# Performance work log

Measured on AMD Instinct MI355X. Metric: run time of the kernel, lower is better.

Reference implementation:

```python
import jax, jax.numpy as jnp
import numpy as np

B, H, W, C = 2, 128, 128, 128
K = 3            # window_size
NB = K * K       # neighbor_count = 9
RP = 8           # relative_position_dim
HID = 128        # edge hidden = max(256//2, 128)
EIN = 3 * C + RP # edge_input_dim = 392
CLIP = 3.0
GEPS = 1e-06     # gate_eps
LNE = 1e-05      # LayerNorm eps


def _ln(x, g, b):
    m = x.mean(-1, keepdims=True)
    v = ((x - m) ** 2).mean(-1, keepdims=True)
    return (x - m) * jax.lax.rsqrt(v + LNE) * g + b


def setup_inputs() -> dict:
    key = jax.random.key(0)
    ks = jax.random.split(key, 12)
    f32 = jnp.float32
    inp = {
        'tokens': jax.random.normal(ks[0], (B, H, W, C), dtype=f32),
        'ln1_g': jnp.ones((C,), f32), 'ln1_b': jnp.zeros((C,), f32),
        'ln2_g': jnp.ones((C,), f32), 'ln2_b': jnp.zeros((C,), f32),
        'rel_pos': 0.02 * jax.random.normal(ks[1], (NB, RP), dtype=f32),
        'dW1': 0.01 * jax.random.normal(ks[2], (EIN, HID), dtype=f32),
        'db1': jnp.zeros((HID,), f32),
        'dW2': 0.01 * jax.random.normal(ks[3], (HID, 1), dtype=f32),
        'db2': jnp.zeros((1,), f32),
        'rW1': 0.01 * jax.random.normal(ks[4], (EIN, HID), dtype=f32),
        'rb1': jnp.zeros((HID,), f32),
        'rW2': 0.01 * jax.random.normal(ks[5], (HID, 1), dtype=f32),
        'rb2': jnp.zeros((1,), f32),
        'vW': 0.01 * jax.random.normal(ks[6], (C, C), dtype=f32),
        'vb': jnp.zeros((C,), f32),
        'oW': 0.01 * jax.random.normal(ks[7], (C, C), dtype=f32),
        'ob': jnp.zeros((C,), f32),
        'eml_gamma': jnp.asarray(0.1, f32),
        'eml_lam': jnp.asarray(1.0, f32),
        'eml_bias': jnp.asarray(-0.3, f32),
    }
    return inp


def _edge_mlp(x, W1, b1, W2, b2):
    h = jax.nn.gelu(jnp.einsum('blnd,dh->blnh', x, W1) + b1, approximate=False)
    return jnp.einsum('blnh,ho->blno', h, W2) + b2


def _forward(tokens, ln1_g, ln1_b, ln2_g, ln2_b, rel_pos, dW1, db1, dW2, db2,
             rW1, rb1, rW2, rb2, vW, vb, oW, ob, eml_gamma, eml_lam, eml_bias,
             warmup_eta=1.0):
    Bh, Hh, Wh, Ch = tokens.shape
    L = Hh * Wh
    normalized = _ln(tokens, ln1_g, ln1_b)
    flat = normalized.reshape(Bh, L, Ch)
    # Unfold(kernel=3, padding=1): gather 9 shifted views, then replicate torch's
    # reshape of the (C, 9)-ordered channel axis into (9, C).
    pad = jnp.pad(normalized, ((0, 0), (1, 1), (1, 1), (0, 0)))
    shifts = [pad[:, i:i + Hh, j:j + Wh, :] for i in range(K) for j in range(K)]
    nbhd = jnp.stack(shifts, axis=-1)                       # [B,H,W,C,9]
    nbhd = nbhd.reshape(Bh, L, Ch * NB).reshape(Bh, L, NB, Ch)  # torch reshape semantics
    center = jnp.broadcast_to(flat[:, :, None, :], nbhd.shape)
    rel = jnp.broadcast_to(rel_pos[None, None], (Bh, L, NB, rel_pos.shape[-1]))
    edge_features = jnp.concatenate([center, nbhd, center - nbhd, rel], axis=-1)
    drive = _edge_mlp(edge_features, dW1, db1, dW2, db2)[..., 0]        # [B,L,9]
    resistance = _edge_mlp(edge_features, rW1, rb1, rW2, rb2)[..., 0]   # [B,L,9]
    # EML unit (Ohm's-law style gate): clamp(eta*gamma*drive/(lambda*softplus(R)+eps)+bias)
    energy = jnp.clip(
        warmup_eta * (eml_gamma * drive) / (eml_lam * jax.nn.softplus(resistance) + GEPS)
        + eml_bias, -CLIP, CLIP)
    gate = jax.nn.sigmoid(energy)                                        # [B,L,9]
    values = jnp.einsum('blnc,cd->blnd', nbhd, vW) + vb                  # [B,L,9,C]
    gate_mass = jnp.maximum(gate.sum(axis=2), GEPS)                      # [B,L]
    message = jnp.einsum('bln,blnc->blc', gate, values) / gate_mass[..., None]
    update = (jnp.einsum('blc,cd->bld', message, oW) + ob).reshape(Bh, Hh, Wh, Ch)
    output = _ln(tokens + update, ln2_g, ln2_b)  # dropout is identity at eval
    return output


def reference(tokens, ln1_g, ln1_b, ln2_g, ln2_b, rel_pos, dW1, db1, dW2, db2,
              rW1, rb1, rW2, rb2, vW, vb, oW, ob, eml_gamma, eml_lam, eml_bias):
    return _forward(tokens, ln1_g, ln1_b, ln2_g, ln2_b, rel_pos, dW1, db1, dW2, db2,
                    rW1, rb1, rW2, rb2, vW, vb, oW, ob, eml_gamma, eml_lam, eml_bias)
```

## Files before the change

### kernel.cpp

```cpp
#include <hip/hip_runtime.h>


#define USHORT unsigned short
#define AW 152

typedef __attribute__((ext_vector_type(8)))  __bf16 v8bf;
typedef __attribute__((ext_vector_type(8)))  USHORT v8u;
typedef __attribute__((ext_vector_type(16))) float  v16f;

__device__ __forceinline__ USHORT f2bf(float f) {
    unsigned v; __builtin_memcpy(&v, &f, 4);
    v += 0x7FFFu + ((v >> 16) & 1u);
    return (USHORT)(v >> 16);
}

__global__ __launch_bounds__(256) void k_setup(
    const float* __restrict__ tok, const float* __restrict__ ln1g,
    const float* __restrict__ ln1b,
    const float* __restrict__ dW1, const float* __restrict__ db1,
    const float* __restrict__ rW1, const float* __restrict__ rb1,
    const float* __restrict__ rel, const float* __restrict__ dW2,
    const float* __restrict__ rW2, const float* __restrict__ vW,
    const float* __restrict__ vb,  const float* __restrict__ oW,
    USHORT* __restrict__ norm,
    USHORT* __restrict__ WnTg, USHORT* __restrict__ WcTg, USHORT* __restrict__ VTg,
    float* __restrict__ preg, float* __restrict__ vboWg, float* __restrict__ w2g)
{
    const int blk = blockIdx.x, t = threadIdx.x;
    if (blk >= 354) {
        const int p = (blk - 354) * 4 + (t >> 6);
        const int lane = t & 63;
        const float2 x = ((const float2*)(tok + (size_t)p * 128))[lane];
        float s = x.x + x.y;
        for (int m = 1; m < 64; m <<= 1) s += __shfl_xor(s, m);
        const float mean = s * (1.f / 128.f);
        const float d0 = x.x - mean, d1 = x.y - mean;
        float q = d0 * d0 + d1 * d1;
        for (int m = 1; m < 64; m <<= 1) q += __shfl_xor(q, m);
        const float rstd = rsqrtf(q * (1.f / 128.f) + 1e-5f);
        const float2 gg = ((const float2*)ln1g)[lane], bb = ((const float2*)ln1b)[lane];
        ((unsigned*)norm)[(size_t)p * 64 + lane] =
            (unsigned)f2bf(d0 * rstd * gg.x + bb.x) |
            ((unsigned)f2bf(d1 * rstd * gg.y + bb.y) << 16);
        return;
    }
    if (blk < 72) {
        int idx = blk * 256 + t;
        int n = ((idx >> 4) * 7282) >> 16;
        int k = idx - n * 144;
        int r = k >> 4, tt = k & 15, c2 = r + 9 * tt;
        float acc = 0.f;
        if (c2 < 128)
            for (int j = 0; j < 128; ++j) acc += vW[c2 * 128 + j] * oW[j * 128 + n];
        VTg[idx] = f2bf(acc);
    } else if (blk < 216) {
        int idx = (blk - 72) * 256 + t;
        int n = ((idx >> 4) * 7282) >> 16;
        int k = idx - n * 144;
        int r = k >> 4, tt = k & 15, c2 = r + 9 * tt;
        int col = n & 127;
        const float* W = (n < 128) ? dW1 : rW1;
        float val = 0.f;
        if (c2 < 128) val = W[(128 + c2) * 128 + col] - W[(256 + c2) * 128 + col];
        WnTg[idx] = f2bf(val);
    } else if (blk < 344) {
        int idx = (blk - 216) * 256 + t;
        int n = idx >> 7, c = idx & 127, col = n & 127;
        const float* W = (n < 128) ? dW1 : rW1;
        WcTg[idx] = f2bf(W[c * 128 + col] + W[(256 + c) * 128 + col]);
    } else if (blk < 353) {
        int n2 = blk - 344; int h = t;
        float acc;
        if (h < 128) {
            acc = db1[h];
            for (int r = 0; r < 8; ++r) acc += rel[n2 * 8 + r] * dW1[(384 + r) * 128 + h];
        } else {
            int hh = h - 128;
            acc = rb1[hh];
            for (int r = 0; r < 8; ++r) acc += rel[n2 * 8 + r] * rW1[(384 + r) * 128 + hh];
        }
        preg[n2 * 256 + h] = acc;
    } else {
        if (t < 128) {
            float acc = 0.f;
            for (int j = 0; j < 128; ++j) acc += vb[j] * oW[j * 128 + t];
            vboWg[t] = acc;
            w2g[t] = dW2[t];
            w2g[128 + t] = rW2[t];
        }
    }
}

__device__ __forceinline__ void gather_tile(
    USHORT* __restrict__ Ash, const USHORT* __restrict__ nb,
    int n2, int y, int bI, int tid)
{
    const int x = tid >> 2, q = tid & 3;
    #pragma unroll
    for (int r = 0; r < 9; ++r) {
        int u = 2 * n2 + r;
        int n = (u >= 18) ? (u - 18) : ((u >= 9) ? (u - 9) : u);
        int v = n2 * 128 + r;
        int c0 = (v * 7282) >> 16;
        int dyq = (n * 22) >> 6;
        int dx = n - 3 * dyq - 1;
        int dy = dyq - 1;
        int sy = y + dy, sx = x + dx;
        bool ok = ((unsigned)sy < 128u) && ((unsigned)sx < 128u);
        int e0 = (c0 & ~1) + 4 * q;
        size_t gidx = ((size_t)((bI * 128 + (ok ? sy : 0)) * 128 + (ok ? sx : 0))) * 128 + e0;
        const unsigned* gp = (const unsigned*)nb + (gidx >> 1);
        unsigned dw0 = gp[0], dw1 = gp[1];
        unsigned nxt = (unsigned)__shfl_down((int)dw0, 1);
        unsigned o0, o1;
        if (c0 & 1) { o0 = (dw0 >> 16) | (dw1 << 16); o1 = (dw1 >> 16) | (nxt << 16); }
        else        { o0 = dw0;                       o1 = dw1; }
        if (!ok) { o0 = 0u; o1 = 0u; }
        *(uint2*)(Ash + x * AW + 16 * r + 4 * q) = make_uint2(o0, o1);
    }
}

__global__ __launch_bounds__(512, 2) void k_edge(
    const float* __restrict__ tok, const float* __restrict__ ln2g,
    const float* __restrict__ ln2b, const USHORT* __restrict__ nb,
    const USHORT* __restrict__ WnTg, const USHORT* __restrict__ WcTg,
    const USHORT* __restrict__ VTg, const float* __restrict__ preg,
    const float* __restrict__ vboWg, const float* __restrict__ w2g,
    const float* __restrict__ db2p, const float* __restrict__ rb2p,
    const float* __restrict__ gmp, const float* __restrict__ lmp,
    const float* __restrict__ bip, const float* __restrict__ obp,
    float* __restrict__ out)
{
    extern __shared__ char smem[];
    USHORT* Wsh  = (USHORT*)smem;
    USHORT* Ash  = (USHORT*)(smem + 77824);
    USHORT* VTl  = (USHORT*)(smem + 116736);
    float*  w2L  = (float*)(smem + 155648);
    float*  dsum = (float*)(smem + 156672);
    float*  rsum = (float*)(smem + 157184);
    float*  gateL= (float*)(smem + 157696);
    float*  sgL  = (float*)(smem + 158208);
    float*  updF = (float*)smem;

    const int tid = threadIdx.x;
    const int lane = tid & 63, wave = tid >> 6, hi = lane >> 5, l31 = lane & 31;
    const int mw = wave & 1, nw = wave >> 1;
    const int blk = blockIdx.x;
    const int bI = blk >> 7;
    const int y = ((blk & 7) << 4) | ((blk >> 3) & 15);
    const int p0 = (bI * 128 + y) * 128;

    for (int i = tid; i < 4096; i += 512) {
        int n = i >> 4, kv = i & 15;
        *(v8u*)(Wsh + n * AW + kv * 8) = *(const v8u*)(WcTg + n * 128 + kv * 8);
    }
    for (int i = tid; i < 2048; i += 512) {
        int x = i >> 4, kv = i & 15;
        *(v8u*)(Ash + x * AW + kv * 8) = *(const v8u*)(nb + (size_t)(p0 + x) * 128 + kv * 8);
    }
    for (int i = tid; i < 2304; i += 512) {
        int n = (i * 3641) >> 16;
        int kv = i - n * 18;
        *(v8u*)(VTl + n * AW + kv * 8) = *(const v8u*)(VTg + n * 144 + kv * 8);
    }
    if (tid < 256) w2L[tid] = w2g[tid];
    if (tid < 128) { dsum[tid] = 0.f; rsum[tid] = 0.f; sgL[tid] = 0.f; }
    __syncthreads();

    v16f cp[2][2];
    #pragma unroll
    for (int a = 0; a < 2; ++a)
        for (int b = 0; b < 2; ++b)
            for (int e = 0; e < 16; ++e) cp[a][b][e] = 0.f;
    #pragma unroll
    for (int ks = 0; ks < 8; ++ks) {
        v8bf af0 = *(const v8bf*)(Ash + (mw * 64 + l31) * AW + ks * 16 + hi * 8);
        v8bf af1 = *(const v8bf*)(Ash + (mw * 64 + 32 + l31) * AW + ks * 16 + hi * 8);
        v8bf bf0 = *(const v8bf*)(Wsh + (nw * 64 + l31) * AW + ks * 16 + hi * 8);
        v8bf bf1 = *(const v8bf*)(Wsh + (nw * 64 + 32 + l31) * AW + ks * 16 + hi * 8);
        cp[0][0] = __builtin_amdgcn_mfma_f32_32x32x16_bf16(af0, bf0, cp[0][0], 0, 0, 0);
        cp[0][1] = __builtin_amdgcn_mfma_f32_32x32x16_bf16(af0, bf1, cp[0][1], 0, 0, 0);
        cp[1][0] = __builtin_amdgcn_mfma_f32_32x32x16_bf16(af1, bf0, cp[1][0], 0, 0, 0);
        cp[1][1] = __builtin_amdgcn_mfma_f32_32x32x16_bf16(af1, bf1, cp[1][1], 0, 0, 0);
    }
    __syncthreads();

    for (int i = tid; i < 4608; i += 512) {
        int n = (i * 3641) >> 16;
        int kv = i - n * 18;
        *(v8u*)(Wsh + n * AW + kv * 8) = *(const v8u*)(WnTg + n * 144 + kv * 8);
    }
    gather_tile(Ash, nb, 0, y, bI, tid);

    const float gmv = gmp[0], lmv = lmp[0], biv = bip[0];
    const float db2v = db2p[0], rb2v = rb2p[0];
    const float wv0 = w2L[nw * 64 + l31];
    const float wv1 = w2L[nw * 64 + 32 + l31];

    v16f acc3[2];
    #pragma unroll
    for (int a = 0; a < 2; ++a)
        for (int e = 0; e < 16; ++e) acc3[a][e] = 0.f;

    for (int n2 = 0; n2 < 9; ++n2) {
        const float pv0 = preg[n2 * 256 + nw * 64 + l31];
        const float pv1 = preg[n2 * 256 + nw * 64 + 32 + l31];
        __syncthreads();
        v16f acc[2][2];
        #pragma unroll
        for (int a = 0; a < 2; ++a)
            for (int b = 0; b < 2; ++b) acc[a][b] = cp[a][b];
        #pragma unroll
        for (int ks = 0; ks < 9; ++ks) {
            v8bf af0 = *(const v8bf*)(Ash + (mw * 64 + l31) * AW + ks * 16 + hi * 8);
            v8bf af1 = *(const v8bf*)(Ash + (mw * 64 + 32 + l31) * AW + ks * 16 + hi * 8);
            v8bf bf0 = *(const v8bf*)(Wsh + (nw * 64 + l31) * AW + ks * 16 + hi * 8);
            v8bf bf1 = *(const v8bf*)(Wsh + (nw * 64 + 32 + l31) * AW + ks * 16 + hi * 8);
            acc[0][0] = __builtin_amdgcn_mfma_f32_32x32x16_bf16(af0, bf0, acc[0][0], 0, 0, 0);
            acc[0][1] = __builtin_amdgcn_mfma_f32_32x32x16_bf16(af0, bf1, acc[0][1], 0, 0, 0);
            acc[1][0] = __builtin_amdgcn_mfma_f32_32x32x16_bf16(af1, bf0, acc[1][0], 0, 0, 0);
            acc[1][1] = __builtin_amdgcn_mfma_f32_32x32x16_bf16(af1, bf1, acc[1][1], 0, 0, 0);
        }
        #pragma unroll
        for (int mt = 0; mt < 2; ++mt) {
            float part[16];
            #pragma unroll
            for (int rr = 0; rr < 16; ++rr) {
                float h0 = acc[mt][0][rr] + pv0;
                float h1 = acc[mt][1][rr] + pv1;
                float s0 = __builtin_amdgcn_rcpf(1.f + __expf(-1.702f * h0));
                float s1 = __builtin_amdgcn_rcpf(1.f + __expf(-1.702f * h1));
                part[rr] = h0 * s0 * wv0 + h1 * s1 * wv1;
            }
            #pragma unroll
            for (int m = 1; m < 32; m <<= 1) {
                #pragma unroll
                for (int rr = 0; rr < 16; ++rr) part[rr] += __shfl_xor(part[rr], m);
            }
            if (l31 == 0) {
                float* tgt = (nw < 2) ? dsum : rsum;
                #pragma unroll
                for (int rr = 0; rr < 16; ++rr) {
                    int row = mw * 64 + mt * 32 + (rr & 3) + 8 * (rr >> 2) + 4 * hi;
                    atomicAdd(&tgt[row], part[rr]);
                }
            }
        }
        v16f P[2];
        #pragma unroll
        for (int a = 0; a < 2; ++a)
            for (int e = 0; e < 16; ++e) P[a][e] = 0.f;
        #pragma unroll
        for (int ks = 0; ks < 9; ++ks) {
            v8bf af0 = *(const v8bf*)(Ash + (mw * 64 + l31) * AW + ks * 16 + hi * 8);
            v8bf af1 = *(const v8bf*)(Ash + (mw * 64 + 32 + l31) * AW + ks * 16 + hi * 8);
            v8bf vf  = *(const v8bf*)(VTl + (nw * 32 + l31) * AW + ks * 16 + hi * 8);
            P[0] = __builtin_amdgcn_mfma_f32_32x32x16_bf16(af0, vf, P[0], 0, 0, 0);
            P[1] = __builtin_amdgcn_mfma_f32_32x32x16_bf16(af1, vf, P[1], 0, 0, 0);
        }
        __syncthreads();
        if (n2 < 8) gather_tile(Ash, nb, n2 + 1, y, bI, tid);
        if (tid < 128) {
            float d = dsum[tid] + db2v, rr = rsum[tid] + rb2v;
            float sp = fmaxf(rr, 0.f) + log1pf(__expf(-fabsf(rr)));
            float e = gmv * d / (lmv * sp + 1e-6f) + biv;
            e = fminf(fmaxf(e, -3.f), 3.f);
            float gt = 1.f / (1.f + __expf(-e));
            gateL[tid] = gt; sgL[tid] += gt;
            dsum[tid] = 0.f; rsum[tid] = 0.f;
        }
        __syncthreads();
        #pragma unroll
        for (int mt = 0; mt < 2; ++mt) {
            const float4* gq = (const float4*)&gateL[mw * 64 + mt * 32 + 4 * hi];
            float4 ga = gq[0], gb = gq[2], gc = gq[4], gd = gq[6];
            float gs[16] = {ga.x, ga.y, ga.z, ga.w, gb.x, gb.y, gb.z, gb.w,
                            gc.x, gc.y, gc.z, gc.w, gd.x, gd.y, gd.z, gd.w};
            #pragma unroll
            for (int rr = 0; rr < 16; ++rr) acc3[mt][rr] += gs[rr] * P[mt][rr];
        }
    }

    if (tid < 128) {
        float s = sgL[tid];
        float m = fmaxf(s, 1e-6f);
        dsum[tid] = 1.f / m;
        rsum[tid] = s / m;
    }
    __syncthreads();

    {
        const int colc = nw * 32 + l31;
        const float vbw = vboWg[colc], obv = obp[colc];
        #pragma unroll
        for (int mt = 0; mt < 2; ++mt) {
            const int base = mw * 64 + mt * 32 + 4 * hi;
            const float4* iq = (const float4*)&dsum[base];
            const float4* sq = (const float4*)&rsum[base];
            float4 ia = iq[0], ib = iq[2], ic = iq[4], id = iq[6];
            float4 sa = sq[0], sb = sq[2], sc = sq[4], sd = sq[6];
            float iv[16] = {ia.x, ia.y, ia.z, ia.w, ib.x, ib.y, ib.z, ib.w,
                            ic.x, ic.y, ic.z, ic.w, id.x, id.y, id.z, id.w};
            float sv[16] = {sa.x, sa.y, sa.z, sa.w, sb.x, sb.y, sb.z, sb.w,
                            sc.x, sc.y, sc.z, sc.w, sd.x, sd.y, sd.z, sd.w};
            #pragma unroll
            for (int rr = 0; rr < 16; ++rr) {
                int row = base + (rr & 3) + 8 * (rr >> 2);
                updF[row * 128 + colc] = acc3[mt][rr] * iv[rr] + vbw * sv[rr] + obv;
            }
        }
    }
    __syncthreads();

    const float g20 = ln2g[lane], g21 = ln2g[lane + 64];
    const float b20 = ln2b[lane], b21 = ln2b[lane + 64];
    for (int q2 = 0; q2 < 16; ++q2) {
        int p = wave * 16 + q2;
        size_t gp = (size_t)(p0 + p) * 128;
        float x0 = tok[gp + lane]      + updF[p * 128 + lane];
        float x1 = tok[gp + lane + 64] + updF[p * 128 + lane + 64];
        float s = x0 + x1;
        for (int m = 1; m < 64; m <<= 1) s += __shfl_xor(s, m);
        float mean = s * (1.f / 128.f);
        float d0 = x0 - mean, d1 = x1 - mean;
        float qq = d0 * d0 + d1 * d1;
        for (int m = 1; m < 64; m <<= 1) qq += __shfl_xor(qq, m);
        float rstd = rsqrtf(qq * (1.f / 128.f) + 1e-5f);
        out[gp + lane]      = d0 * rstd * g20 + b20;
        out[gp + lane + 64] = d1 * rstd * g21 + b21;
    }
}

extern "C" void kernel_launch(void* const* d_in, const int* in_sizes, int n_in,
                              void* d_out, int out_size, void* d_ws, size_t ws_size,
                              hipStream_t stream) {
    const float* tok  = (const float*)d_in[0];
    const float* ln1g = (const float*)d_in[1];
    const float* ln1b = (const float*)d_in[2];
    const float* ln2g = (const float*)d_in[3];
    const float* ln2b = (const float*)d_in[4];
    const float* rel  = (const float*)d_in[5];
    const float* dW1  = (const float*)d_in[6];
    const float* db1  = (const float*)d_in[7];
    const float* dW2  = (const float*)d_in[8];
    const float* db2  = (const float*)d_in[9];
    const float* rW1  = (const float*)d_in[10];
    const float* rb1  = (const float*)d_in[11];
    const float* rW2  = (const float*)d_in[12];
    const float* rb2  = (const float*)d_in[13];
    const float* vW   = (const float*)d_in[14];
    const float* vb   = (const float*)d_in[15];
    const float* oW   = (const float*)d_in[16];
    const float* ob   = (const float*)d_in[17];
    const float* gm   = (const float*)d_in[18];
    const float* lm   = (const float*)d_in[19];
    const float* bi   = (const float*)d_in[20];
    float* out = (float*)d_out;

    char* w = (char*)d_ws;
    USHORT* norm = (USHORT*)w; w += 8388608;
    USHORT* WnTg = (USHORT*)w; w += 73728;
    USHORT* WcTg = (USHORT*)w; w += 65536;
    USHORT* VTg  = (USHORT*)w; w += 36864;
    float*  preg = (float*)w;  w += 9216;
    float*  vboWg= (float*)w;  w += 512;
    float*  w2g  = (float*)w;  w += 1024;

    hipFuncSetAttribute((const void*)k_edge,
                        hipFuncAttributeMaxDynamicSharedMemorySize, 158720);

    hipLaunchKernelGGL(k_setup, dim3(8546), dim3(256), 0, stream,
                       tok, ln1g, ln1b, dW1, db1, rW1, rb1, rel, dW2, rW2,
                       vW, vb, oW, norm, WnTg, WcTg, VTg, preg, vboWg, w2g);
    hipLaunchKernelGGL(k_edge, dim3(256), dim3(512), 158720, stream,
                       tok, ln2g, ln2b, norm, WnTg, WcTg, VTg, preg, vboWg, w2g,
                       db2, rb2, gm, lm, bi, ob, out);
}
```

Before: 209.8 us.

## Double edge kernel workgroup to 1024 threads and fuse value GEMM into edge loop

The edge kernel now runs 16 waves per workgroup with 32x32 output tiles per wave. Each wave computes the drive, resistance and value MFMAs in one pass over a combined weight buffer in shared memory. Sums are double-buffered, which removes one barrier per neighbor step, and the next neighbor gather is loaded into registers before the barrier so it overlaps compute. The setup kernel is reorganised so that more threads are active and it zero-fills the padding slots. The change adds more atomics per row and lowers per-wave register headroom, and occupancy is limited by the roughly 155KB of shared memory per workgroup.

```diff
diff --git a/kernel.cpp b/kernel.cpp
--- a/kernel.cpp
+++ b/kernel.cpp
@@ -8,6 +8,12 @@
 typedef __attribute__((ext_vector_type(8)))  USHORT v8u;
 typedef __attribute__((ext_vector_type(16))) float  v16f;
 
+__device__ __forceinline__ float bflo(unsigned u) {
+    unsigned v = u << 16; float f; __builtin_memcpy(&f, &v, 4); return f;
+}
+__device__ __forceinline__ float bfhi(unsigned u) {
+    unsigned v = u & 0xffff0000u; float f; __builtin_memcpy(&f, &v, 4); return f;
+}
 __device__ __forceinline__ USHORT f2bf(float f) {
     unsigned v; __builtin_memcpy(&v, &f, 4);
     v += 0x7FFFu + ((v >> 16) & 1u);
@@ -27,8 +33,8 @@
     float* __restrict__ preg, float* __restrict__ vboWg, float* __restrict__ w2g)
 {
     const int blk = blockIdx.x, t = threadIdx.x;
-    if (blk >= 354) {
-        const int p = (blk - 354) * 4 + (t >> 6);
+    if (blk < 8192) {
+        const int p = blk * 4 + (t >> 6);
         const int lane = t & 63;
         const float2 x = ((const float2*)(tok + (size_t)p * 128))[lane];
         float s = x.x + x.y;
@@ -44,32 +50,28 @@
             ((unsigned)f2bf(d1 * rstd * gg.y + bb.y) << 16);
         return;
     }
-    if (blk < 72) {
-        int idx = blk * 256 + t;
-        int n = ((idx >> 4) * 7282) >> 16;
-        int k = idx - n * 144;
-        int r = k >> 4, tt = k & 15, c2 = r + 9 * tt;
+    const int b2 = blk - 8192;
+    if (b2 < 64) {
+        int c2 = b2 * 2 + (t >> 7);
+        int n = t & 127;
         float acc = 0.f;
-        if (c2 < 128)
-            for (int j = 0; j < 128; ++j) acc += vW[c2 * 128 + j] * oW[j * 128 + n];
-        VTg[idx] = f2bf(acc);
-    } else if (blk < 216) {
-        int idx = (blk - 72) * 256 + t;
-        int n = ((idx >> 4) * 7282) >> 16;
-        int k = idx - n * 144;
-        int r = k >> 4, tt = k & 15, c2 = r + 9 * tt;
-        int col = n & 127;
+        for (int j = 0; j < 128; ++j) acc += vW[c2 * 128 + j] * oW[j * 128 + n];
+        int tt = (c2 * 7282) >> 16, r = c2 - 9 * tt;
+        VTg[n * 144 + 16 * r + tt] = f2bf(acc);
+    } else if (b2 < 192) {
+        int c2 = b2 - 64;
+        int n = t, col = t & 127;
         const float* W = (n < 128) ? dW1 : rW1;
-        float val = 0.f;
-        if (c2 < 128) val = W[(128 + c2) * 128 + col] - W[(256 + c2) * 128 + col];
-        WnTg[idx] = f2bf(val);
-    } else if (blk < 344) {
-        int idx = (blk - 216) * 256 + t;
-        int n = idx >> 7, c = idx & 127, col = n & 127;
+        float val = W[(128 + c2) * 128 + col] - W[(256 + c2) * 128 + col];
+        int tt = (c2 * 7282) >> 16, r = c2 - 9 * tt;
+        WnTg[n * 144 + 16 * r + tt] = f2bf(val);
+    } else if (b2 < 320) {
+        int c = b2 - 192;
+        int n = t, col = t & 127;
         const float* W = (n < 128) ? dW1 : rW1;
-        WcTg[idx] = f2bf(W[c * 128 + col] + W[(256 + c) * 128 + col]);
-    } else if (blk < 353) {
-        int n2 = blk - 344; int h = t;
+        WcTg[n * 128 + c] = f2bf(W[c * 128 + col] + W[(256 + c) * 128 + col]);
+    } else if (b2 < 329) {
+        int n2 = b2 - 320; int h = t;
         float acc;
         if (h < 128) {
             acc = db1[h];
@@ -80,7 +82,7 @@
             for (int r = 0; r < 8; ++r) acc += rel[n2 * 8 + r] * rW1[(384 + r) * 128 + hh];
         }
         preg[n2 * 256 + h] = acc;
-    } else {
+    } else if (b2 == 329) {
         if (t < 128) {
             float acc = 0.f;
             for (int j = 0; j < 128; ++j) acc += vb[j] * oW[j * 128 + t];
@@ -88,14 +90,26 @@
             w2g[t] = dW2[t];
             w2g[128 + t] = rW2[t];
         }
-    }
-}
-
-__device__ __forceinline__ void gather_tile(
-    USHORT* __restrict__ Ash, const USHORT* __restrict__ nb,
-    int n2, int y, int bI, int tid)
+    } else {
+        for (int i = t; i < 2048; i += 256) {
+            int n = i >> 4, j = i & 15;
+            int slot = (j == 0) ? 15 : (j == 1) ? 31
+                      : 16 * (2 + ((j - 2) >> 1)) + 14 + ((j - 2) & 1);
+            VTg[n * 144 + slot] = 0;
+        }
+        for (int i = t; i < 4096; i += 256) {
+            int n = i >> 4, j = i & 15;
+            int slot = (j == 0) ? 15 : (j == 1) ? 31
+                      : 16 * (2 + ((j - 2) >> 1)) + 14 + ((j - 2) & 1);
+            WnTg[n * 144 + slot] = 0;
+        }
+    }
+}
+
+__device__ __forceinline__ void gather_load(
+    unsigned gv[9], const USHORT* __restrict__ nb,
+    int n2, int y, int bI, int x, int q)
 {
-    const int x = tid >> 2, q = tid & 3;
     #pragma unroll
     for (int r = 0; r < 9; ++r) {
         int u = 2 * n2 + r;
@@ -103,24 +117,26 @@
         int v = n2 * 128 + r;
         int c0 = (v * 7282) >> 16;
         int dyq = (n * 22) >> 6;
-        int dx = n - 3 * dyq - 1;
-        int dy = dyq - 1;
+        int dx = n - 3 * dyq - 1, dy = dyq - 1;
         int sy = y + dy, sx = x + dx;
         bool ok = ((unsigned)sy < 128u) && ((unsigned)sx < 128u);
-        int e0 = (c0 & ~1) + 4 * q;
+        int e0 = (c0 & ~1) + 2 * q;
         size_t gidx = ((size_t)((bI * 128 + (ok ? sy : 0)) * 128 + (ok ? sx : 0))) * 128 + e0;
-        const unsigned* gp = (const unsigned*)nb + (gidx >> 1);
-        unsigned dw0 = gp[0], dw1 = gp[1];
-        unsigned nxt = (unsigned)__shfl_down((int)dw0, 1);
-        unsigned o0, o1;
-        if (c0 & 1) { o0 = (dw0 >> 16) | (dw1 << 16); o1 = (dw1 >> 16) | (nxt << 16); }
-        else        { o0 = dw0;                       o1 = dw1; }
-        if (!ok) { o0 = 0u; o1 = 0u; }
-        *(uint2*)(Ash + x * AW + 16 * r + 4 * q) = make_uint2(o0, o1);
-    }
-}
-
-__global__ __launch_bounds__(512, 2) void k_edge(
+        unsigned dw = ((const unsigned*)nb)[gidx >> 1];
+        unsigned nxt = (unsigned)__shfl_down((int)dw, 1);
+        unsigned o = (c0 & 1) ? ((dw >> 16) | (nxt << 16)) : dw;
+        gv[r] = ok ? o : 0u;
+    }
+}
+__device__ __forceinline__ void gather_store(
+    USHORT* __restrict__ Ash, const unsigned gv[9], int x, int q)
+{
+    #pragma unroll
+    for (int r = 0; r < 9; ++r)
+        *(unsigned*)(Ash + x * AW + 16 * r + 2 * q) = gv[r];
+}
+
+__global__ __launch_bounds__(1024, 4) void k_edge(
     const float* __restrict__ tok, const float* __restrict__ ln2g,
     const float* __restrict__ ln2b, const USHORT* __restrict__ nb,
     const USHORT* __restrict__ WnTg, const USHORT* __restrict__ WcTg,
@@ -132,190 +148,166 @@
     float* __restrict__ out)
 {
     extern __shared__ char smem[];
-    USHORT* Wsh  = (USHORT*)smem;
-    USHORT* Ash  = (USHORT*)(smem + 77824);
-    USHORT* VTl  = (USHORT*)(smem + 116736);
-    float*  w2L  = (float*)(smem + 155648);
-    float*  dsum = (float*)(smem + 156672);
-    float*  rsum = (float*)(smem + 157184);
-    float*  gateL= (float*)(smem + 157696);
-    float*  sgL  = (float*)(smem + 158208);
+    USHORT* Wp   = (USHORT*)smem;
+    USHORT* Ash  = (USHORT*)(smem + 116736);
+    float*  sums = (float*)(smem + 155648);
+    float*  sgL  = sums + 512;
     float*  updF = (float*)smem;
 
     const int tid = threadIdx.x;
     const int lane = tid & 63, wave = tid >> 6, hi = lane >> 5, l31 = lane & 31;
-    const int mw = wave & 1, nw = wave >> 1;
+    const int mw = wave & 3, nw = wave >> 2;
+    const int gx = tid >> 3, gq = tid & 7;
     const int blk = blockIdx.x;
     const int bI = blk >> 7;
     const int y = ((blk & 7) << 4) | ((blk >> 3) & 15);
     const int p0 = (bI * 128 + y) * 128;
 
-    for (int i = tid; i < 4096; i += 512) {
+    for (int i = tid; i < 4096; i += 1024) {
         int n = i >> 4, kv = i & 15;
-        *(v8u*)(Wsh + n * AW + kv * 8) = *(const v8u*)(WcTg + n * 128 + kv * 8);
-    }
-    for (int i = tid; i < 2048; i += 512) {
+        *(v8u*)(Wp + n * AW + kv * 8) = *(const v8u*)(WcTg + n * 128 + kv * 8);
+    }
+    for (int i = tid; i < 2048; i += 1024) {
         int x = i >> 4, kv = i & 15;
         *(v8u*)(Ash + x * AW + kv * 8) = *(const v8u*)(nb + (size_t)(p0 + x) * 128 + kv * 8);
     }
-    for (int i = tid; i < 2304; i += 512) {
+    if (tid < 640) sums[tid] = 0.f;
+    __syncthreads();
+
+    v16f c0a, c1a;
+    #pragma unroll
+    for (int e = 0; e < 16; ++e) { c0a[e] = 0.f; c1a[e] = 0.f; }
+    #pragma unroll
+    for (int ks = 0; ks < 8; ++ks) {
+        v8bf a  = *(const v8bf*)(Ash + (mw * 32 + l31) * AW + ks * 16 + hi * 8);
+        v8bf b0 = *(const v8bf*)(Wp + (nw * 32 + l31) * AW + ks * 16 + hi * 8);
+        v8bf b1 = *(const v8bf*)(Wp + (128 + nw * 32 + l31) * AW + ks * 16 + hi * 8);
+        c0a = __builtin_amdgcn_mfma_f32_32x32x16_bf16(a, b0, c0a, 0, 0, 0);
+        c1a = __builtin_amdgcn_mfma_f32_32x32x16_bf16(a, b1, c1a, 0, 0, 0);
+    }
+    unsigned cpk[16];
+    #pragma unroll
+    for (int e = 0; e < 16; ++e)
+        cpk[e] = (unsigned)f2bf(c0a[e]) | ((unsigned)f2bf(c1a[e]) << 16);
+    __syncthreads();
+
+    for (int i = tid; i < 6912; i += 1024) {
         int n = (i * 3641) >> 16;
         int kv = i - n * 18;
-        *(v8u*)(VTl + n * AW + kv * 8) = *(const v8u*)(VTg + n * 144 + kv * 8);
-    }
-    if (tid < 256) w2L[tid] = w2g[tid];
-    if (tid < 128) { dsum[tid] = 0.f; rsum[tid] = 0.f; sgL[tid] = 0.f; }
-    __syncthreads();
-
-    v16f cp[2][2];
-    #pragma unroll
-    for (int a = 0; a < 2; ++a)
-        for (int b = 0; b < 2; ++b)
-            for (int e = 0; e < 16; ++e) cp[a][b][e] = 0.f;
-    #pragma unroll
-    for (int ks = 0; ks < 8; ++ks) {
-        v8bf af0 = *(const v8bf*)(Ash + (mw * 64 + l31) * AW + ks * 16 + hi * 8);
-        v8bf af1 = *(const v8bf*)(Ash + (mw * 64 + 32 + l31) * AW + ks * 16 + hi * 8);
-        v8bf bf0 = *(const v8bf*)(Wsh + (nw * 64 + l31) * AW + ks * 16 + hi * 8);
-        v8bf bf1 = *(const v8bf*)(Wsh + (nw * 64 + 32 + l31) * AW + ks * 16 + hi * 8);
-        cp[0][0] = __builtin_amdgcn_mfma_f32_32x32x16_bf16(af0, bf0, cp[0][0], 0, 0, 0);
-        cp[0][1] = __builtin_amdgcn_mfma_f32_32x32x16_bf16(af0, bf1, cp[0][1], 0, 0, 0);
-        cp[1][0] = __builtin_amdgcn_mfma_f32_32x32x16_bf16(af1, bf0, cp[1][0], 0, 0, 0);
-        cp[1][1] = __builtin_amdgcn_mfma_f32_32x32x16_bf16(af1, bf1, cp[1][1], 0, 0, 0);
-    }
-    __syncthreads();
-
-    for (int i = tid; i < 4608; i += 512) {
-        int n = (i * 3641) >> 16;
-        int kv = i - n * 18;
-        *(v8u*)(Wsh + n * AW + kv * 8) = *(const v8u*)(WnTg + n * 144 + kv * 8);
-    }
-    gather_tile(Ash, nb, 0, y, bI, tid);
+        const USHORT* src = (n < 256) ? (WnTg + n * 144 + kv * 8)
+                                      : (VTg + (n - 256) * 144 + kv * 8);
+        *(v8u*)(Wp + n * AW + kv * 8) = *(const v8u*)src;
+    }
+    {
+        unsigned gv[9];
+        gather_load(gv, nb, 0, y, bI, gx, gq);
+        gather_store(Ash, gv, gx, gq);
+    }
+    __syncthreads();
 
     const float gmv = gmp[0], lmv = lmp[0], biv = bip[0];
     const float db2v = db2p[0], rb2v = rb2p[0];
-    const float wv0 = w2L[nw * 64 + l31];
-    const float wv1 = w2L[nw * 64 + 32 + l31];
-
-    v16f acc3[2];
-    #pragma unroll
-    for (int a = 0; a < 2; ++a)
-        for (int e = 0; e < 16; ++e) acc3[a][e] = 0.f;
+    const float w2d = w2g[nw * 32 + l31];
+    const float w2r = w2g[128 + nw * 32 + l31];
+    const USHORT* Ar = Ash + (mw * 32 + l31) * AW;
+    const USHORT* Bd = Wp + (nw * 32 + l31) * AW;
+    const USHORT* Br = Wp + (128 + nw * 32 + l31) * AW;
+    const USHORT* Bm = Wp + (256 + nw * 32 + l31) * AW;
+
+    v16f acc3;
+    #pragma unroll
+    for (int e = 0; e < 16; ++e) acc3[e] = 0.f;
 
     for (int n2 = 0; n2 < 9; ++n2) {
-        const float pv0 = preg[n2 * 256 + nw * 64 + l31];
-        const float pv1 = preg[n2 * 256 + nw * 64 + 32 + l31];
-        __syncthreads();
-        v16f acc[2][2];
-        #pragma unroll
-        for (int a = 0; a < 2; ++a)
-            for (int b = 0; b < 2; ++b) acc[a][b] = cp[a][b];
+        const float pre_d = preg[n2 * 256 + nw * 32 + l31];
+        const float pre_r = preg[n2 * 256 + 128 + nw * 32 + l31];
+        float* ds = sums + (n2 & 1) * 256;
+        float* rs = ds + 128;
+        float* dz = sums + ((n2 & 1) ^ 1) * 256;
+
+        v16f ad, ar, am;
+        #pragma unroll
+        for (int e = 0; e < 16; ++e) { ad[e] = 0.f; ar[e] = 0.f; am[e] = 0.f; }
         #pragma unroll
         for (int ks = 0; ks < 9; ++ks) {
-            v8bf af0 = *(const v8bf*)(Ash + (mw * 64 + l31) * AW + ks * 16 + hi * 8);
-            v8bf af1 = *(const v8bf*)(Ash + (mw * 64 + 32 + l31) * AW + ks * 16 + hi * 8);
-            v8bf bf0 = *(const v8bf*)(Wsh + (nw * 64 + l31) * AW + ks * 16 + hi * 8);
-            v8bf bf1 = *(const v8bf*)(Wsh + (nw * 64 + 32 + l31) * AW + ks * 16 + hi * 8);
-            acc[0][0] = __builtin_amdgcn_mfma_f32_32x32x16_bf16(af0, bf0, acc[0][0], 0, 0, 0);
-            acc[0][1] = __builtin_amdgcn_mfma_f32_32x32x16_bf16(af0, bf1, acc[0][1], 0, 0, 0);
-            acc[1][0] = __builtin_amdgcn_mfma_f32_32x32x16_bf16(af1, bf0, acc[1][0], 0, 0, 0);
-            acc[1][1] = __builtin_amdgcn_mfma_f32_32x32x16_bf16(af1, bf1, acc[1][1], 0, 0, 0);
-        }
-        #pragma unroll
-        for (int mt = 0; mt < 2; ++mt) {
-            float part[16];
+            v8bf a  = *(const v8bf*)(Ar + ks * 16 + hi * 8);
+            v8bf b0 = *(const v8bf*)(Bd + ks * 16 + hi * 8);
+            v8bf b1 = *(const v8bf*)(Br + ks * 16 + hi * 8);
+            v8bf b2 = *(const v8bf*)(Bm + ks * 16 + hi * 8);
+            ad = __builtin_amdgcn_mfma_f32_32x32x16_bf16(a, b0, ad, 0, 0, 0);
+            ar = __builtin_amdgcn_mfma_f32_32x32x16_bf16(a, b1, ar, 0, 0, 0);
+            am = __builtin_amdgcn_mfma_f32_32x32x16_bf16(a, b2, am, 0, 0, 0);
+        }
+
+        float z[16];
+        #pragma unroll
+        for (int rr = 0; rr < 16; ++rr) {
+            float h0 = ad[rr] + pre_d + bflo(cpk[rr]);
+            float h1 = ar[rr] + pre_r + bfhi(cpk[rr]);
+            float p0v = h0 * __builtin_amdgcn_rcpf(1.f + __expf(-1.702f * h0)) * w2d;
+            float p1v = h1 * __builtin_amdgcn_rcpf(1.f + __expf(-1.702f * h1)) * w2r;
+            float sa = p0v + __shfl_xor(p0v, 1);
+            float sb = p1v + __shfl_xor(p1v, 1);
+            z[rr] = (l31 & 1) ? sb : sa;
+        }
+        #pragma unroll
+        for (int m = 2; m < 32; m <<= 1) {
+            #pragma unroll
+            for (int rr = 0; rr < 16; ++rr) z[rr] += __shfl_xor(z[rr], m);
+        }
+        if (l31 < 2) {
+            float* tgt = (l31 == 0) ? ds : rs;
             #pragma unroll
             for (int rr = 0; rr < 16; ++rr) {
-                float h0 = acc[mt][0][rr] + pv0;
-                float h1 = acc[mt][1][rr] + pv1;
-                float s0 = __builtin_amdgcn_rcpf(1.f + __expf(-1.702f * h0));
-                float s1 = __builtin_amdgcn_rcpf(1.f + __expf(-1.702f * h1));
-                part[rr] = h0 * s0 * wv0 + h1 * s1 * wv1;
+                int row = mw * 32 + (rr & 3) + 8 * (rr >> 2) + 4 * hi;
+                atomicAdd(&tgt[row], z[rr]);
             }
-            #pragma unroll
-            for (int m = 1; m < 32; m <<= 1) {
-                #pragma unroll
-                for (int rr = 0; rr < 16; ++rr) part[rr] += __shfl_xor(part[rr], m);
-            }
-            if (l31 == 0) {
-                float* tgt = (nw < 2) ? dsum : rsum;
-                #pragma unroll
-                for (int rr = 0; rr < 16; ++rr) {
-                    int row = mw * 64 + mt * 32 + (rr & 3) + 8 * (rr >> 2) + 4 * hi;
-                    atomicAdd(&tgt[row], part[rr]);
-                }
-            }
-        }
-        v16f P[2];
-        #pragma unroll
-        for (int a = 0; a < 2; ++a)
-            for (int e = 0; e < 16; ++e) P[a][e] = 0.f;
-        #pragma unroll
-        for (int ks = 0; ks < 9; ++ks) {
-            v8bf af0 = *(const v8bf*)(Ash + (mw * 64 + l31) * AW + ks * 16 + hi * 8);
-            v8bf af1 = *(const v8bf*)(Ash + (mw * 64 + 32 + l31) * AW + ks * 16 + hi * 8);
-            v8bf vf  = *(const v8bf*)(VTl + (nw * 32 + l31) * AW + ks * 16 + hi * 8);
-            P[0] = __builtin_amdgcn_mfma_f32_32x32x16_bf16(af0, vf, P[0], 0, 0, 0);
-            P[1] = __builtin_amdgcn_mfma_f32_32x32x16_bf16(af1, vf, P[1], 0, 0, 0);
-        }
+        }
+
+        unsigned gv[9];
+        if (n2 < 8) gather_load(gv, nb, n2 + 1, y, bI, gx, gq);
+
         __syncthreads();
-        if (n2 < 8) gather_tile(Ash, nb, n2 + 1, y, bI, tid);
-        if (tid < 128) {
-            float d = dsum[tid] + db2v, rr = rsum[tid] + rb2v;
-            float sp = fmaxf(rr, 0.f) + log1pf(__expf(-fabsf(rr)));
+
+        if (n2 < 8) gather_store(Ash, gv, gx, gq);
+
+        #pragma unroll
+        for (int rr = 0; rr < 16; ++rr) {
+            int row = mw * 32 + (rr & 3) + 8 * (rr >> 2) + 4 * hi;
+            float d = ds[row] + db2v, r = rs[row] + rb2v;
+            float sp = fmaxf(r, 0.f) + log1pf(__expf(-fabsf(r)));
             float e = gmv * d / (lmv * sp + 1e-6f) + biv;
             e = fminf(fmaxf(e, -3.f), 3.f);
             float gt = 1.f / (1.f + __expf(-e));
-            gateL[tid] = gt; sgL[tid] += gt;
-            dsum[tid] = 0.f; rsum[tid] = 0.f;
-        }
+            acc3[rr] += gt * am[rr];
+            if (nw == 0 && l31 == 0) sgL[row] += gt;
+        }
+        if (tid < 256) dz[tid] = 0.f;
         __syncthreads();
-        #pragma unroll
-        for (int mt = 0; mt < 2; ++mt) {
-            const float4* gq = (const float4*)&gateL[mw * 64 + mt * 32 + 4 * hi];
-            float4 ga = gq[0], gb = gq[2], gc = gq[4], gd = gq[6];
-            float gs[16] = {ga.x, ga.y, ga.z, ga.w, gb.x, gb.y, gb.z, gb.w,
-                            gc.x, gc.y, gc.z, gc.w, gd.x, gd.y, gd.z, gd.w};
-            #pragma unroll
-            for (int rr = 0; rr < 16; ++rr) acc3[mt][rr] += gs[rr] * P[mt][rr];
-        }
     }
 
     if (tid < 128) {
         float s = sgL[tid];
         float m = fmaxf(s, 1e-6f);
-        dsum[tid] = 1.f / m;
-        rsum[tid] = s / m;
-    }
-    __syncthreads();
-
+        sums[tid] = 1.f / m;
+        sums[128 + tid] = s / m;
+    }
+    __syncthreads();
     {
-        const int colc = nw * 32 + l31;
-        const float vbw = vboWg[colc], obv = obp[colc];
-        #pragma unroll
-        for (int mt = 0; mt < 2; ++mt) {
-            const int base = mw * 64 + mt * 32 + 4 * hi;
-            const float4* iq = (const float4*)&dsum[base];
-            const float4* sq = (const float4*)&rsum[base];
-            float4 ia = iq[0], ib = iq[2], ic = iq[4], id = iq[6];
-            float4 sa = sq[0], sb = sq[2], sc = sq[4], sd = sq[6];
-            float iv[16] = {ia.x, ia.y, ia.z, ia.w, ib.x, ib.y, ib.z, ib.w,
-                            ic.x, ic.y, ic.z, ic.w, id.x, id.y, id.z, id.w};
-            float sv[16] = {sa.x, sa.y, sa.z, sa.w, sb.x, sb.y, sb.z, sb.w,
-                            sc.x, sc.y, sc.z, sc.w, sd.x, sd.y, sd.z, sd.w};
-            #pragma unroll
-            for (int rr = 0; rr < 16; ++rr) {
-                int row = base + (rr & 3) + 8 * (rr >> 2);
-                updF[row * 128 + colc] = acc3[mt][rr] * iv[rr] + vbw * sv[rr] + obv;
-            }
+        const int col = nw * 32 + l31;
+        const float vbw = vboWg[col], obv = obp[col];
+        #pragma unroll
+        for (int rr = 0; rr < 16; ++rr) {
+            int row = mw * 32 + (rr & 3) + 8 * (rr >> 2) + 4 * hi;
+            updF[row * 128 + col] = acc3[rr] * sums[row] + vbw * sums[128 + row] + obv;
         }
     }
     __syncthreads();
 
     const float g20 = ln2g[lane], g21 = ln2g[lane + 64];
     const float b20 = ln2b[lane], b21 = ln2b[lane + 64];
-    for (int q2 = 0; q2 < 16; ++q2) {
-        int p = wave * 16 + q2;
+    for (int q2 = 0; q2 < 8; ++q2) {
+        int p = wave * 8 + q2;
         size_t gp = (size_t)(p0 + p) * 128;
         float x0 = tok[gp + lane]      + updF[p * 128 + lane];
         float x1 = tok[gp + lane + 64] + updF[p * 128 + lane + 64];
@@ -367,12 +359,12 @@
     float*  w2g  = (float*)w;  w += 1024;
 
     hipFuncSetAttribute((const void*)k_edge,
-                        hipFuncAttributeMaxDynamicSharedMemorySize, 158720);
-
-    hipLaunchKernelGGL(k_setup, dim3(8546), dim3(256), 0, stream,
+                        hipFuncAttributeMaxDynamicSharedMemorySize, 158208);
+
+    hipLaunchKernelGGL(k_setup, dim3(8523), dim3(256), 0, stream,
                        tok, ln1g, ln1b, dW1, db1, rW1, rb1, rel, dW2, rW2,
                        vW, vb, oW, norm, WnTg, WcTg, VTg, preg, vboWg, w2g);
-    hipLaunchKernelGGL(k_edge, dim3(256), dim3(512), 158720, stream,
+    hipLaunchKernelGGL(k_edge, dim3(256), dim3(1024), 158208, stream,
                        tok, ln2g, ln2b, norm, WnTg, WcTg, VTg, preg, vboWg, w2g,
                        db2, rb2, gm, lm, bi, ob, out);
 }
```

After: 411.7 us. 1.96x slower.
